# Performance work log

Hardware: AMD Instinct MI355X
Metric: run time of the kernel (lower is better)

## Reference

```python
import jax, jax.numpy as jnp
import numpy as np
import math

B, T, D, H = 4, 2048, 512, 8
MAX_LEN = 2048
DK = D // H


def setup_inputs() -> dict:
    key = jax.random.key(0)
    ks = jax.random.split(key, 12)
    s = 0.02
    inp = {
        "x": jax.random.normal(ks[0], (B, T, D), dtype=jnp.float32),
        "mask": jax.random.bernoulli(ks[1], 0.85, (B, T)),  # True = observed
        "Wq": jax.random.normal(ks[2], (D, D), dtype=jnp.float32) * s,
        "bq": jnp.zeros((D,), dtype=jnp.float32),
        "Wk": jax.random.normal(ks[3], (D, D), dtype=jnp.float32) * s,
        "bk": jnp.zeros((D,), dtype=jnp.float32),
        "Wv": jax.random.normal(ks[4], (D, D), dtype=jnp.float32) * s,
        "bv": jnp.zeros((D,), dtype=jnp.float32),
        "Wo": jax.random.normal(ks[5], (D, D), dtype=jnp.float32) * s,
        "bo": jnp.zeros((D,), dtype=jnp.float32),
        "missing_bias": jnp.zeros((1, H, 1, 1), dtype=jnp.float32),
        "rel_pos_embed": jax.random.normal(ks[6], (2 * MAX_LEN - 1, H), dtype=jnp.float32) * 0.01,
    }
    return inp


def _sinusoidal_pe(t, d):
    pos = jnp.arange(t, dtype=jnp.float32)[:, None]                      # [T,1]
    div = jnp.exp(jnp.arange(0, d, 2, dtype=jnp.float32) * (-math.log(10000.0) / d))
    pe = jnp.zeros((t, d), dtype=jnp.float32)
    pe = pe.at[:, 0::2].set(jnp.sin(pos * div))
    pe = pe.at[:, 1::2].set(jnp.cos(pos * div))
    return pe


def _attention(x, mask, Wq, bq, Wk, bk, Wv, bv, Wo, bo, missing_bias, rel_pos_embed):
    b, t, d = x.shape
    h = missing_bias.shape[1]
    dk = d // h
    max_len = (rel_pos_embed.shape[0] + 1) // 2

    x = x + _sinusoidal_pe(t, d)[None]

    def proj(w, bias):  # [B,T,D] -> [B,H,T,dk]
        y = jnp.einsum('btd,ed->bte', x, w) + bias
        return y.reshape(b, t, h, dk).transpose(0, 2, 1, 3)

    Q, K, V = proj(Wq, bq), proj(Wk, bk), proj(Wv, bv)

    scores = jnp.einsum('bhqd,bhkd->bhqk', Q, K) / math.sqrt(dk)  # [B,H,T,T]

    # relative position bias, antisymmetrized
    pos = jnp.arange(t)
    rel_idx = pos[:, None] - pos[None, :] + (max_len - 1)          # [T,T]
    bias = rel_pos_embed[rel_idx]                                  # [T,T,H]
    bias = 0.5 * (bias - bias.transpose(1, 0, 2))
    scores = scores + bias.transpose(2, 0, 1)[None]                # [B,H,T,T]

    # missing-token masking on keys: -inf fill then add missing_bias at masked spots
    m = mask[:, None, None, :]                                     # [B,1,1,T]
    scores = jnp.where(m, scores, -jnp.inf)
    scores = jnp.where(m, scores, scores + missing_bias)

    attn = jax.nn.softmax(scores, axis=-1)
    out = jnp.einsum('bhqk,bhkd->bhqd', attn, V)
    out = out.transpose(0, 2, 1, 3).reshape(b, t, d)
    return jnp.einsum('btd,ed->bte', out, Wo) + bo


def reference(x, mask, Wq, bq, Wk, bk, Wv, bv, Wo, bo, missing_bias, rel_pos_embed):
    return _attention(x, mask, Wq, bq, Wk, bk, Wv, bv, Wo, bo, missing_bias, rel_pos_embed)
```

## Files before the change

kernel.cpp:

```cpp
#include <hip/hip_runtime.h>

#define B_ 4
#define T_ 2048
#define D_ 512
#define H_ 8
#define DK_ 64
#define TBL 4095

typedef __attribute__((ext_vector_type(4))) float f32x4;
typedef __attribute__((ext_vector_type(8))) short bf16x8;
typedef __attribute__((ext_vector_type(4))) int i32x4;
typedef unsigned int u32;

static __device__ __forceinline__ float b2f(ushort u) {
    union { float f; unsigned int i; } c;
    c.i = ((unsigned int)u) << 16;
    return c.f;
}

static __device__ __forceinline__ ushort f2b(float f) {
    union { float f; unsigned int i; } c;
    c.f = f;
    unsigned int i = c.i;
    unsigned int r = (i + 0x7fffu + ((i >> 16) & 1u)) >> 16;
    return (ushort)r;
}

static __device__ __forceinline__ void gload_lds16(const void* g, void* l) {
    __builtin_amdgcn_global_load_lds(
        (const __attribute__((address_space(1))) u32*)g,
        (__attribute__((address_space(3))) u32*)(u32)(unsigned long long)l,
        16, 0, 0);
}

__global__ __launch_bounds__(64) void detect_mask_kernel(const unsigned int* __restrict__ mask,
                                                         int* __restrict__ flags) {
    int lane = threadIdx.x;
    int c2 = 0, c1 = 0;
    for (int i = lane; i < 512; i += 64) {
        unsigned int v = mask[i];
        c2 += (v == 0x3F803F80u || v == 0x00010001u) ? 1 : 0;
        c1 += (v == 0x01010101u) ? 1 : 0;
    }
#pragma unroll
    for (int m = 1; m < 64; m <<= 1) {
        c2 += __shfl_xor(c2, m);
        c1 += __shfl_xor(c1, m);
    }
    if (lane == 0) flags[0] = (c2 > 8) ? 2 : ((c1 > 8) ? 1 : 0);
}

__global__ __launch_bounds__(256) void mask_prep_kernel(const void* __restrict__ mask,
                                                        const int* __restrict__ flags,
                                                        int* __restrict__ maskw) {
    int j = blockIdx.x * 256 + threadIdx.x;
    int fm = flags[0];
    int v;
    if (fm == 2)      v = (((const ushort*)mask)[j] != 0);
    else if (fm == 1) v = (((const unsigned char*)mask)[j] != 0);
    else              v = (((const int*)mask)[j] != 0);
    maskw[j] = v;
}

__global__ __launch_bounds__(256) void wcvt_kernel(
    const float* __restrict__ W0, const float* __restrict__ W1,
    const float* __restrict__ W2, const float* __restrict__ W3,
    ushort* __restrict__ Wc) {
    const int z = blockIdx.z;
    const float* Ws = (z == 0) ? W0 : ((z == 1) ? W1 : ((z == 2) ? W2 : W3));
    int idx = blockIdx.x * 256 + threadIdx.x;
    const float* wf = Ws + idx * 8;
    f32x4 a = *(const f32x4*)(wf);
    f32x4 c = *(const f32x4*)(wf + 4);
    union { ushort u[8]; i32x4 v; } o;
#pragma unroll
    for (int j = 0; j < 4; ++j) { o.u[j] = f2b(a[j]); o.u[4 + j] = f2b(c[j]); }
    *(i32x4*)(Wc + (size_t)z * (D_ * D_) + idx * 8) = o.v;
}

__global__ __launch_bounds__(256) void pe_kernel(const float* __restrict__ x,
                                                 ushort* __restrict__ xp) {
    int idx = blockIdx.x * 256 + threadIdx.x;
    int i = idx & 255;
    int row = idx >> 8;
    int t = row & (T_ - 1);
    float div = __expf((float)i * -0.035977892f);
    float ang = (float)t * div;
    float s = sinf(ang);
    float c = cosf(ang);
    float2 v = ((const float2*)x)[row * 256 + i];
    unsigned int o = (unsigned int)f2b(v.x + s) | ((unsigned int)f2b(v.y + c) << 16);
    *(unsigned int*)(xp + (size_t)row * D_ + 2 * i) = o;
}

__global__ __launch_bounds__(256) void bias_tbl_kernel(const float* __restrict__ E,
                                                       float* __restrict__ tbl) {
    int idx = blockIdx.x * 256 + threadIdx.x;
    if (idx >= TBL * H_) return;
    int h = idx & 7;
    int j = idx >> 3;
    tbl[(size_t)h * TBL + j] =
        0.72134752044f * (E[(size_t)j * H_ + h] - E[(size_t)(4094 - j) * H_ + h]);
}

template <int OUTMODE>
__global__ __launch_bounds__(256) void gemm_bt_kernel(
    const ushort* __restrict__ A,
    const ushort* __restrict__ W0, const ushort* __restrict__ W1, const ushort* __restrict__ W2,
    const float* __restrict__ bias0, const float* __restrict__ bias1, const float* __restrict__ bias2,
    void* __restrict__ O0, void* __restrict__ O1, void* __restrict__ O2) {
    __shared__ ushort As[128 * 32];
    __shared__ ushort Bs[128 * 32];

    const int z = blockIdx.z;
    const ushort* Wp = (z == 0) ? W0 : ((z == 1) ? W1 : W2);
    const float* bp = (z == 0) ? bias0 : ((z == 1) ? bias1 : bias2);
    void* Op = (z == 0) ? O0 : ((z == 1) ? O1 : O2);

    const int n0 = blockIdx.x * 128;
    const int m0 = blockIdx.y * 128;
    const int tid = threadIdx.x;
    const int lane = tid & 63;
    const int w = tid >> 6;
    const int wr = (w >> 1) * 64;
    const int wc = (w & 1) * 64;
    const int l15 = lane & 15;
    const int lg = lane >> 4;

    f32x4 acc[4][4];
#pragma unroll
    for (int mi = 0; mi < 4; ++mi)
#pragma unroll
        for (int ni = 0; ni < 4; ++ni)
            acc[mi][ni] = (f32x4){0.f, 0.f, 0.f, 0.f};

    for (int kt = 0; kt < D_ / 32; ++kt) {
#pragma unroll
        for (int p = 0; p < 2; ++p) {
            int c = tid + p * 256;
            int r = c >> 2;
            int s = c & 3;
            gload_lds16(A  + (size_t)(m0 + r) * D_ + kt * 32 + s * 8, As + c * 8);
            gload_lds16(Wp + (size_t)(n0 + r) * D_ + kt * 32 + s * 8, Bs + c * 8);
        }
        __syncthreads();

        bf16x8 af[4], bfr[4];
#pragma unroll
        for (int mi = 0; mi < 4; ++mi)
            af[mi] = *(const bf16x8*)(As + (wr + mi * 16 + l15) * 32 + lg * 8);
#pragma unroll
        for (int ni = 0; ni < 4; ++ni)
            bfr[ni] = *(const bf16x8*)(Bs + (wc + ni * 16 + l15) * 32 + lg * 8);
#pragma unroll
        for (int mi = 0; mi < 4; ++mi)
#pragma unroll
            for (int ni = 0; ni < 4; ++ni)
                acc[mi][ni] = __builtin_amdgcn_mfma_f32_16x16x32_bf16(af[mi], bfr[ni], acc[mi][ni], 0, 0, 0);
        __syncthreads();
    }

#pragma unroll
    for (int ni = 0; ni < 4; ++ni) {
        int n = n0 + wc + ni * 16 + l15;
        float bv = bp[n];
#pragma unroll
        for (int mi = 0; mi < 4; ++mi) {
#pragma unroll
            for (int i = 0; i < 4; ++i) {
                int m = m0 + wr + mi * 16 + lg * 4 + i;
                float v = acc[mi][ni][i] + bv;
                if (OUTMODE == 0) {
                    int b = m >> 11;
                    int t = m & 2047;
                    int h = n >> 6;
                    int dk = n & 63;
                    ((ushort*)Op)[(((size_t)(b * H_ + h) * T_ + t) << 6) + dk] = f2b(v);
                } else {
                    ((float*)Op)[(size_t)m * D_ + n] = v;
                }
            }
        }
    }
}

__global__ __launch_bounds__(512) void attn_kernel(
    const ushort* __restrict__ Q, const ushort* __restrict__ K, const ushort* __restrict__ V,
    const int* __restrict__ maskw, const float* __restrict__ tbl,
    ushort* __restrict__ Aout) {
    __shared__ ushort Ks[64 * 64];
    __shared__ ushort Vs[64 * 64];
    __shared__ ushort Ps[8][16 * 64];
    __shared__ float biasl[2176];
    __shared__ float maskl[T_];

    const int qb = blockIdx.x;
    const int bh = blockIdx.y;
    const int b = bh >> 3;
    const int h = bh & 7;
    const int tid = threadIdx.x;
    const int lane = tid & 63;
    const int w = tid >> 6;
    const int l15 = lane & 15;
    const int lg = lane >> 4;

    const ushort* Qp = Q + (size_t)bh * T_ * DK_;
    const ushort* Kp = K + (size_t)bh * T_ * DK_;
    const ushort* Vp = V + (size_t)bh * T_ * DK_;

    for (int j = tid; j < 2176; j += 512) {
        int gj = qb * 128 + j;
        biasl[j] = (gj <= 4094) ? tbl[(size_t)h * TBL + gj] : 0.f;
    }
    for (int j = tid; j < T_; j += 512)
        maskl[j] = (maskw[b * T_ + j] != 0) ? 1.0f : 0.0f;

    const int q0 = qb * 128 + w * 16;
    bf16x8 qf[2];
#pragma unroll
    for (int kf = 0; kf < 2; ++kf)
        qf[kf] = *(const bf16x8*)(Qp + (size_t)(q0 + l15) * DK_ + kf * 32 + lg * 8);

    f32x4 acc[4];
    float rs[4];
#pragma unroll
    for (int ni = 0; ni < 4; ++ni) acc[ni] = (f32x4){0.f, 0.f, 0.f, 0.f};
#pragma unroll
    for (int i = 0; i < 4; ++i) rs[i] = 0.f;
    __syncthreads();

    for (int kt = 0; kt < T_ / 64; ++kt) {
        {
            int r = tid >> 3;
            int sl = tid & 7;
            i32x4 kv = *(const i32x4*)(Kp + (size_t)(kt * 64 + r) * DK_ + ((sl ^ (r & 7)) * 8));
            *(i32x4*)(Ks + tid * 8) = kv;
        }
        {
            int key = tid >> 3;
            int dq = (tid & 7) * 8;
            bf16x8 v = *(const bf16x8*)(Vp + (size_t)(kt * 64 + key) * DK_ + dq);
            const ushort* pv8 = (const ushort*)&v;
#pragma unroll
            for (int j = 0; j < 8; ++j) {
                int dk = dq + j;
                Vs[dk * 64 + (((key >> 3) ^ (dk & 7)) * 8) + (key & 7)] = pv8[j];
            }
        }
        __syncthreads();

#pragma unroll
        for (int ct = 0; ct < 4; ++ct) {
            int krow = ct * 16 + l15;
            bf16x8 kf0 = *(const bf16x8*)(Ks + krow * 64 + ((lg ^ (krow & 7)) * 8));
            bf16x8 kf1 = *(const bf16x8*)(Ks + krow * 64 + (((4 + lg) ^ (krow & 7)) * 8));
            int kg = kt * 64 + ct * 16 + l15;
            float mf = maskl[kg];
            f32x4 S = (f32x4){0.f, 0.f, 0.f, 0.f};
            S = __builtin_amdgcn_mfma_f32_16x16x32_bf16(qf[0], kf0, S, 0, 0, 0);
            S = __builtin_amdgcn_mfma_f32_16x16x32_bf16(qf[1], kf1, S, 0, 0, 0);
            int jb = w * 16 + lg * 4 - kg + 2047;
#pragma unroll
            for (int i = 0; i < 4; ++i) {
                float pv = mf * exp2f(fmaf(S[i], 0.1803368801f, biasl[jb + i]));
                rs[i] += pv;
                int prow = lg * 4 + i;
                int pcol = ct * 16 + l15;
                Ps[w][prow * 64 + (((pcol >> 3) ^ (prow & 7)) * 8) + (pcol & 7)] = f2b(pv);
            }
        }

#pragma unroll
        for (int kk = 0; kk < 2; ++kk) {
            bf16x8 pf = *(const bf16x8*)(Ps[w] + l15 * 64 + (((kk * 4 + lg) ^ (l15 & 7)) * 8));
#pragma unroll
            for (int ni = 0; ni < 4; ++ni) {
                int vrow = ni * 16 + l15;
                bf16x8 vf = *(const bf16x8*)(Vs + vrow * 64 + (((kk * 4 + lg) ^ (vrow & 7)) * 8));
                acc[ni] = __builtin_amdgcn_mfma_f32_16x16x32_bf16(pf, vf, acc[ni], 0, 0, 0);
            }
        }
        __syncthreads();
    }

#pragma unroll
    for (int i = 0; i < 4; ++i) {
        float v = rs[i];
        v += __shfl_xor(v, 1);
        v += __shfl_xor(v, 2);
        v += __shfl_xor(v, 4);
        v += __shfl_xor(v, 8);
        rs[i] = v;
    }

#pragma unroll
    for (int ni = 0; ni < 4; ++ni)
#pragma unroll
        for (int i = 0; i < 4; ++i) {
            int t = q0 + lg * 4 + i;
            int d = h * DK_ + ni * 16 + l15;
            Aout[(size_t)(b * T_ + t) * D_ + d] = f2b(acc[ni][i] / rs[i]);
        }
}

extern "C" void kernel_launch(void* const* d_in, const int* in_sizes, int n_in,
                              void* d_out, int out_size, void* d_ws, size_t ws_size,
                              hipStream_t stream) {
    const float* x   = (const float*)d_in[0];
    const void* mask = d_in[1];
    const float* Wq  = (const float*)d_in[2];
    const float* bq  = (const float*)d_in[3];
    const float* Wk  = (const float*)d_in[4];
    const float* bk  = (const float*)d_in[5];
    const float* Wv  = (const float*)d_in[6];
    const float* bv  = (const float*)d_in[7];
    const float* Wo  = (const float*)d_in[8];
    const float* bo  = (const float*)d_in[9];
    const float* E   = (const float*)d_in[11];
    float* out = (float*)d_out;

    char* ws = (char*)d_ws;
    ushort* xp  = (ushort*)(ws);
    ushort* Qw  = (ushort*)(ws + (8u << 20));
    ushort* Kw  = (ushort*)(ws + (16u << 20));
    ushort* Vw  = (ushort*)(ws + (24u << 20));
    float* tbl  = (float*)(ws + (32u << 20));
    ushort* Wc  = (ushort*)(ws + (32u << 20) + 262144);
    int* maskw  = (int*)(ws + (34u << 20) + 262144);
    int* flags  = (int*)(ws + (34u << 20) + 262144 + 32768);

    if (ws_size < (35u << 20)) return;

    detect_mask_kernel<<<1, 64, 0, stream>>>((const unsigned int*)mask, flags);
    mask_prep_kernel<<<(B_ * T_) / 256, 256, 0, stream>>>(mask, flags, maskw);
    bias_tbl_kernel<<<(TBL * H_ + 255) / 256, 256, 0, stream>>>(E, tbl);
    pe_kernel<<<B_ * T_, 256, 0, stream>>>(x, xp);

    dim3 gw(128, 1, 4);
    wcvt_kernel<<<gw, 256, 0, stream>>>(Wq, Wk, Wv, Wo, Wc);

    dim3 g1(D_ / 128, (B_ * T_) / 128, 3);
    gemm_bt_kernel<0><<<g1, 256, 0, stream>>>(xp, Wc, Wc + D_ * D_, Wc + 2 * D_ * D_,
                                              bq, bk, bv, Qw, Kw, Vw);

    dim3 g2(T_ / 128, B_ * H_, 1);
    attn_kernel<<<g2, 512, 0, stream>>>(Qw, Kw, Vw, maskw, tbl, xp);

    dim3 g3(D_ / 128, (B_ * T_) / 128, 1);
    gemm_bt_kernel<1><<<g3, 256, 0, stream>>>(xp, Wc + 3 * D_ * D_, Wc + 3 * D_ * D_, Wc + 3 * D_ * D_,
                                              bo, bo, bo, out, out, out);
}
```

Baseline: 269.7 us.

## Widen GEMM K-tile with swizzled LDS, shrink attention blocks, async K loads

The projection GEMM now stages 64-wide K tiles with an XOR-swizzled LDS layout, which halves the number of barriers and is meant to reduce bank conflicts. The attention kernel moves from 128-query, 512-thread blocks to 64-query, 256-thread blocks, doubling the grid for better occupancy and load balance. K tiles are loaded with direct global-to-LDS copies, and V is transposed by packing pairs of keys into 32-bit LDS stores. The mask is stored as bf16 to shrink LDS use. The trade-off is that each K/V tile is now reloaded by twice as many blocks.

```diff
diff --git a/kernel.cpp b/kernel.cpp
--- a/kernel.cpp
+++ b/kernel.cpp
@@ -109,8 +109,8 @@
     const ushort* __restrict__ W0, const ushort* __restrict__ W1, const ushort* __restrict__ W2,
     const float* __restrict__ bias0, const float* __restrict__ bias1, const float* __restrict__ bias2,
     void* __restrict__ O0, void* __restrict__ O1, void* __restrict__ O2) {
-    __shared__ ushort As[128 * 32];
-    __shared__ ushort Bs[128 * 32];
+    __shared__ ushort As[128 * 64];
+    __shared__ ushort Bs[128 * 64];
 
     const int z = blockIdx.z;
     const ushort* Wp = (z == 0) ? W0 : ((z == 1) ? W1 : W2);
@@ -134,29 +134,34 @@
         for (int ni = 0; ni < 4; ++ni)
             acc[mi][ni] = (f32x4){0.f, 0.f, 0.f, 0.f};
 
-    for (int kt = 0; kt < D_ / 32; ++kt) {
-#pragma unroll
-        for (int p = 0; p < 2; ++p) {
+    for (int kt = 0; kt < D_ / 64; ++kt) {
+#pragma unroll
+        for (int p = 0; p < 4; ++p) {
             int c = tid + p * 256;
-            int r = c >> 2;
-            int s = c & 3;
-            gload_lds16(A  + (size_t)(m0 + r) * D_ + kt * 32 + s * 8, As + c * 8);
-            gload_lds16(Wp + (size_t)(n0 + r) * D_ + kt * 32 + s * 8, Bs + c * 8);
+            int r = c >> 3;
+            int scol = ((c & 7) ^ (r & 7)) * 8;
+            gload_lds16(A  + (size_t)(m0 + r) * D_ + kt * 64 + scol, As + c * 8);
+            gload_lds16(Wp + (size_t)(n0 + r) * D_ + kt * 64 + scol, Bs + c * 8);
         }
         __syncthreads();
 
-        bf16x8 af[4], bfr[4];
-#pragma unroll
-        for (int mi = 0; mi < 4; ++mi)
-            af[mi] = *(const bf16x8*)(As + (wr + mi * 16 + l15) * 32 + lg * 8);
-#pragma unroll
-        for (int ni = 0; ni < 4; ++ni)
-            bfr[ni] = *(const bf16x8*)(Bs + (wc + ni * 16 + l15) * 32 + lg * 8);
-#pragma unroll
-        for (int mi = 0; mi < 4; ++mi)
+#pragma unroll
+        for (int ks = 0; ks < 2; ++ks) {
+            bf16x8 af[4], bfr[4];
+#pragma unroll
+            for (int mi = 0; mi < 4; ++mi)
+                af[mi] = *(const bf16x8*)(As + (wr + mi * 16 + l15) * 64 +
+                                          (((ks * 4 + lg) ^ (l15 & 7)) * 8));
 #pragma unroll
             for (int ni = 0; ni < 4; ++ni)
-                acc[mi][ni] = __builtin_amdgcn_mfma_f32_16x16x32_bf16(af[mi], bfr[ni], acc[mi][ni], 0, 0, 0);
+                bfr[ni] = *(const bf16x8*)(Bs + (wc + ni * 16 + l15) * 64 +
+                                           (((ks * 4 + lg) ^ (l15 & 7)) * 8));
+#pragma unroll
+            for (int mi = 0; mi < 4; ++mi)
+#pragma unroll
+                for (int ni = 0; ni < 4; ++ni)
+                    acc[mi][ni] = __builtin_amdgcn_mfma_f32_16x16x32_bf16(af[mi], bfr[ni], acc[mi][ni], 0, 0, 0);
+        }
         __syncthreads();
     }
 
@@ -184,15 +189,15 @@
     }
 }
 
-__global__ __launch_bounds__(512) void attn_kernel(
+__global__ __launch_bounds__(256) void attn_kernel(
     const ushort* __restrict__ Q, const ushort* __restrict__ K, const ushort* __restrict__ V,
     const int* __restrict__ maskw, const float* __restrict__ tbl,
     ushort* __restrict__ Aout) {
     __shared__ ushort Ks[64 * 64];
     __shared__ ushort Vs[64 * 64];
-    __shared__ ushort Ps[8][16 * 64];
-    __shared__ float biasl[2176];
-    __shared__ float maskl[T_];
+    __shared__ ushort Ps[4][16 * 64];
+    __shared__ float biasl[2112];
+    __shared__ ushort maskl[T_];
 
     const int qb = blockIdx.x;
     const int bh = blockIdx.y;
@@ -208,14 +213,14 @@
     const ushort* Kp = K + (size_t)bh * T_ * DK_;
     const ushort* Vp = V + (size_t)bh * T_ * DK_;
 
-    for (int j = tid; j < 2176; j += 512) {
-        int gj = qb * 128 + j;
+    for (int j = tid; j < 2112; j += 256) {
+        int gj = qb * 64 + j;
         biasl[j] = (gj <= 4094) ? tbl[(size_t)h * TBL + gj] : 0.f;
     }
-    for (int j = tid; j < T_; j += 512)
-        maskl[j] = (maskw[b * T_ + j] != 0) ? 1.0f : 0.0f;
-
-    const int q0 = qb * 128 + w * 16;
+    for (int j = tid; j < T_; j += 256)
+        maskl[j] = (maskw[b * T_ + j] != 0) ? 0x3F80 : 0;
+
+    const int q0 = qb * 64 + w * 16;
     bf16x8 qf[2];
 #pragma unroll
     for (int kf = 0; kf < 2; ++kf)
@@ -230,21 +235,29 @@
     __syncthreads();
 
     for (int kt = 0; kt < T_ / 64; ++kt) {
+#pragma unroll
+        for (int p = 0; p < 2; ++p) {
+            int c = tid + p * 256;
+            int r = c >> 3;
+            int scol = ((c & 7) ^ (r & 7)) * 8;
+            gload_lds16(Kp + (size_t)(kt * 64 + r) * DK_ + scol, Ks + c * 8);
+        }
         {
-            int r = tid >> 3;
-            int sl = tid & 7;
-            i32x4 kv = *(const i32x4*)(Kp + (size_t)(kt * 64 + r) * DK_ + ((sl ^ (r & 7)) * 8));
-            *(i32x4*)(Ks + tid * 8) = kv;
-        }
-        {
-            int key = tid >> 3;
-            int dq = (tid & 7) * 8;
-            bf16x8 v = *(const bf16x8*)(Vp + (size_t)(kt * 64 + key) * DK_ + dq);
-            const ushort* pv8 = (const ushort*)&v;
+            int p2 = lane & 31;
+            int half = lane >> 5;
+            int dk0 = w * 16 + half * 8;
+            const ushort* src = Vp + (size_t)(kt * 64 + 2 * p2) * DK_ + dk0;
+            i32x4 lo = *(const i32x4*)(src);
+            i32x4 hi = *(const i32x4*)(src + DK_);
+            const ushort* plo = (const ushort*)&lo;
+            const ushort* phi = (const ushort*)&hi;
 #pragma unroll
             for (int j = 0; j < 8; ++j) {
-                int dk = dq + j;
-                Vs[dk * 64 + (((key >> 3) ^ (dk & 7)) * 8) + (key & 7)] = pv8[j];
+                int dk = dk0 + j;
+                unsigned int word = (unsigned int)plo[j] | ((unsigned int)phi[j] << 16);
+                int slot = p2 >> 2;
+                int wi = p2 & 3;
+                *(unsigned int*)(Vs + dk * 64 + ((slot ^ (dk & 7)) * 8) + wi * 2) = word;
             }
         }
         __syncthreads();
@@ -255,7 +268,7 @@
             bf16x8 kf0 = *(const bf16x8*)(Ks + krow * 64 + ((lg ^ (krow & 7)) * 8));
             bf16x8 kf1 = *(const bf16x8*)(Ks + krow * 64 + (((4 + lg) ^ (krow & 7)) * 8));
             int kg = kt * 64 + ct * 16 + l15;
-            float mf = maskl[kg];
+            float mf = b2f(maskl[kg]);
             f32x4 S = (f32x4){0.f, 0.f, 0.f, 0.f};
             S = __builtin_amdgcn_mfma_f32_16x16x32_bf16(qf[0], kf0, S, 0, 0, 0);
             S = __builtin_amdgcn_mfma_f32_16x16x32_bf16(qf[1], kf1, S, 0, 0, 0);
@@ -343,8 +356,8 @@
     gemm_bt_kernel<0><<<g1, 256, 0, stream>>>(xp, Wc, Wc + D_ * D_, Wc + 2 * D_ * D_,
                                               bq, bk, bv, Qw, Kw, Vw);
 
-    dim3 g2(T_ / 128, B_ * H_, 1);
-    attn_kernel<<<g2, 512, 0, stream>>>(Qw, Kw, Vw, maskw, tbl, xp);
+    dim3 g2(T_ / 64, B_ * H_, 1);
+    attn_kernel<<<g2, 256, 0, stream>>>(Qw, Kw, Vw, maskw, tbl, xp);
 
     dim3 g3(D_ / 128, (B_ * T_) / 128, 1);
     gemm_bt_kernel<1><<<g3, 256, 0, stream>>>(xp, Wc + 3 * D_ * D_, Wc + 3 * D_ * D_, Wc + 3 * D_ * D_,
```

Result: faster. 231.7 us (-14.1%).

## Write V transposed from projection GEMM and load K/V tiles via direct LDS loads

Applied to the files above, without the earlier changes.

The QKV projection GEMM now writes V in a [B,H,DK,T] transposed layout, so the attention kernel can fill its V tile with swizzled direct global-to-LDS loads instead of an element-by-element scatter transpose. K loads also switch to gload_lds16. Separately, the GEMM K-tile is doubled to 64 with an XOR swizzle to cut barrier count and LDS bank conflicts, and the mask is stored as bf16 in LDS. The V writes become strided (poorly coalesced) in the GEMM epilogue, which adds store cost there.

```diff
diff --git a/kernel.cpp b/kernel.cpp
--- a/kernel.cpp
+++ b/kernel.cpp
@@ -109,8 +109,8 @@
     const ushort* __restrict__ W0, const ushort* __restrict__ W1, const ushort* __restrict__ W2,
     const float* __restrict__ bias0, const float* __restrict__ bias1, const float* __restrict__ bias2,
     void* __restrict__ O0, void* __restrict__ O1, void* __restrict__ O2) {
-    __shared__ ushort As[128 * 32];
-    __shared__ ushort Bs[128 * 32];
+    __shared__ ushort As[128 * 64];
+    __shared__ ushort Bs[128 * 64];
 
     const int z = blockIdx.z;
     const ushort* Wp = (z == 0) ? W0 : ((z == 1) ? W1 : W2);
@@ -134,29 +134,34 @@
         for (int ni = 0; ni < 4; ++ni)
             acc[mi][ni] = (f32x4){0.f, 0.f, 0.f, 0.f};
 
-    for (int kt = 0; kt < D_ / 32; ++kt) {
-#pragma unroll
-        for (int p = 0; p < 2; ++p) {
+    for (int kt = 0; kt < D_ / 64; ++kt) {
+#pragma unroll
+        for (int p = 0; p < 4; ++p) {
             int c = tid + p * 256;
-            int r = c >> 2;
-            int s = c & 3;
-            gload_lds16(A  + (size_t)(m0 + r) * D_ + kt * 32 + s * 8, As + c * 8);
-            gload_lds16(Wp + (size_t)(n0 + r) * D_ + kt * 32 + s * 8, Bs + c * 8);
+            int r = c >> 3;
+            int scol = ((c & 7) ^ (r & 7)) * 8;
+            gload_lds16(A  + (size_t)(m0 + r) * D_ + kt * 64 + scol, As + c * 8);
+            gload_lds16(Wp + (size_t)(n0 + r) * D_ + kt * 64 + scol, Bs + c * 8);
         }
         __syncthreads();
 
-        bf16x8 af[4], bfr[4];
-#pragma unroll
-        for (int mi = 0; mi < 4; ++mi)
-            af[mi] = *(const bf16x8*)(As + (wr + mi * 16 + l15) * 32 + lg * 8);
-#pragma unroll
-        for (int ni = 0; ni < 4; ++ni)
-            bfr[ni] = *(const bf16x8*)(Bs + (wc + ni * 16 + l15) * 32 + lg * 8);
-#pragma unroll
-        for (int mi = 0; mi < 4; ++mi)
+#pragma unroll
+        for (int ks = 0; ks < 2; ++ks) {
+            bf16x8 af[4], bfr[4];
+#pragma unroll
+            for (int mi = 0; mi < 4; ++mi)
+                af[mi] = *(const bf16x8*)(As + (wr + mi * 16 + l15) * 64 +
+                                          (((ks * 4 + lg) ^ (l15 & 7)) * 8));
 #pragma unroll
             for (int ni = 0; ni < 4; ++ni)
-                acc[mi][ni] = __builtin_amdgcn_mfma_f32_16x16x32_bf16(af[mi], bfr[ni], acc[mi][ni], 0, 0, 0);
+                bfr[ni] = *(const bf16x8*)(Bs + (wc + ni * 16 + l15) * 64 +
+                                           (((ks * 4 + lg) ^ (l15 & 7)) * 8));
+#pragma unroll
+            for (int mi = 0; mi < 4; ++mi)
+#pragma unroll
+                for (int ni = 0; ni < 4; ++ni)
+                    acc[mi][ni] = __builtin_amdgcn_mfma_f32_16x16x32_bf16(af[mi], bfr[ni], acc[mi][ni], 0, 0, 0);
+        }
         __syncthreads();
     }
 
@@ -173,9 +178,12 @@
                 if (OUTMODE == 0) {
                     int b = m >> 11;
                     int t = m & 2047;
-                    int h = n >> 6;
+                    int hh = n >> 6;
                     int dk = n & 63;
-                    ((ushort*)Op)[(((size_t)(b * H_ + h) * T_ + t) << 6) + dk] = f2b(v);
+                    size_t off;
+                    if (z == 2) off = ((size_t)(b * H_ + hh) * DK_ + dk) * T_ + t;
+                    else        off = (((size_t)(b * H_ + hh) * T_ + t) << 6) + dk;
+                    ((ushort*)Op)[off] = f2b(v);
                 } else {
                     ((float*)Op)[(size_t)m * D_ + n] = v;
                 }
@@ -185,14 +193,14 @@
 }
 
 __global__ __launch_bounds__(512) void attn_kernel(
-    const ushort* __restrict__ Q, const ushort* __restrict__ K, const ushort* __restrict__ V,
+    const ushort* __restrict__ Q, const ushort* __restrict__ K, const ushort* __restrict__ Vt,
     const int* __restrict__ maskw, const float* __restrict__ tbl,
     ushort* __restrict__ Aout) {
     __shared__ ushort Ks[64 * 64];
     __shared__ ushort Vs[64 * 64];
     __shared__ ushort Ps[8][16 * 64];
     __shared__ float biasl[2176];
-    __shared__ float maskl[T_];
+    __shared__ ushort maskl[T_];
 
     const int qb = blockIdx.x;
     const int bh = blockIdx.y;
@@ -206,14 +214,14 @@
 
     const ushort* Qp = Q + (size_t)bh * T_ * DK_;
     const ushort* Kp = K + (size_t)bh * T_ * DK_;
-    const ushort* Vp = V + (size_t)bh * T_ * DK_;
+    const ushort* Vp = Vt + (size_t)bh * DK_ * T_;
 
     for (int j = tid; j < 2176; j += 512) {
         int gj = qb * 128 + j;
         biasl[j] = (gj <= 4094) ? tbl[(size_t)h * TBL + gj] : 0.f;
     }
     for (int j = tid; j < T_; j += 512)
-        maskl[j] = (maskw[b * T_ + j] != 0) ? 1.0f : 0.0f;
+        maskl[j] = (maskw[b * T_ + j] != 0) ? 0x3F80 : 0;
 
     const int q0 = qb * 128 + w * 16;
     bf16x8 qf[2];
@@ -232,20 +240,9 @@
     for (int kt = 0; kt < T_ / 64; ++kt) {
         {
             int r = tid >> 3;
-            int sl = tid & 7;
-            i32x4 kv = *(const i32x4*)(Kp + (size_t)(kt * 64 + r) * DK_ + ((sl ^ (r & 7)) * 8));
-            *(i32x4*)(Ks + tid * 8) = kv;
-        }
-        {
-            int key = tid >> 3;
-            int dq = (tid & 7) * 8;
-            bf16x8 v = *(const bf16x8*)(Vp + (size_t)(kt * 64 + key) * DK_ + dq);
-            const ushort* pv8 = (const ushort*)&v;
-#pragma unroll
-            for (int j = 0; j < 8; ++j) {
-                int dk = dq + j;
-                Vs[dk * 64 + (((key >> 3) ^ (dk & 7)) * 8) + (key & 7)] = pv8[j];
-            }
+            int scol = ((tid & 7) ^ (r & 7)) * 8;
+            gload_lds16(Kp + (size_t)(kt * 64 + r) * DK_ + scol, Ks + tid * 8);
+            gload_lds16(Vp + (size_t)r * T_ + kt * 64 + scol, Vs + tid * 8);
         }
         __syncthreads();
 
@@ -255,7 +252,7 @@
             bf16x8 kf0 = *(const bf16x8*)(Ks + krow * 64 + ((lg ^ (krow & 7)) * 8));
             bf16x8 kf1 = *(const bf16x8*)(Ks + krow * 64 + (((4 + lg) ^ (krow & 7)) * 8));
             int kg = kt * 64 + ct * 16 + l15;
-            float mf = maskl[kg];
+            float mf = b2f(maskl[kg]);
             f32x4 S = (f32x4){0.f, 0.f, 0.f, 0.f};
             S = __builtin_amdgcn_mfma_f32_16x16x32_bf16(qf[0], kf0, S, 0, 0, 0);
             S = __builtin_amdgcn_mfma_f32_16x16x32_bf16(qf[1], kf1, S, 0, 0, 0);
```

Result: faster. 231.1 us (-14.3%).
